# Optimization experiments

Hardware: AMD Instinct MI355X
Metric: run time of the kernel (lower is better)

Reference implementation:

```python
import jax, jax.numpy as jnp
import numpy as np

B, S, D, H, O = 8, 4096, 512, 512, 512
NS, NC, SD = 4, 4, 8
CLIP, TEMP, SUP_SCALE, SUP_EPS, LN_EPS = 3.0, 1.0, 1.0, 1e-4, 1e-5


def _ln(x, w, b):
    m = jnp.mean(x, -1, keepdims=True)
    v = jnp.mean((x - m) ** 2, -1, keepdims=True)
    return (x - m) * jax.lax.rsqrt(v + LN_EPS) * w + b


def _lin(x, w, b):
    return x @ w.T + b


def setup_inputs() -> dict:
    key = jax.random.key(0)
    ks = iter(jax.random.split(key, 32))

    def W(shape):
        return 0.02 * jax.random.normal(next(ks), shape, jnp.float32)

    inp = {}
    inp['x'] = jax.random.normal(next(ks), (B, S, D), jnp.float32)
    inp['sb_norm_w'] = jnp.ones((D,), jnp.float32)
    inp['sb_norm_b'] = jnp.zeros((D,), jnp.float32)
    inp['sb_proj_w'] = W((NS, D)); inp['sb_proj_b'] = jnp.zeros((NS,), jnp.float32)
    inp['sb_sum_w'] = W((SD, 4)); inp['sb_sum_b'] = jnp.zeros((SD,), jnp.float32)
    inp['cb_norm_w'] = jnp.ones((D,), jnp.float32)
    inp['cb_norm_b'] = jnp.zeros((D,), jnp.float32)
    inp['cb_proj_w'] = W((NC, D)); inp['cb_proj_b'] = jnp.zeros((NC,), jnp.float32)
    inp['cb_sum_w'] = W((SD, 4)); inp['cb_sum_b'] = jnp.zeros((SD,), jnp.float32)
    inp['vn_norm_w'] = jnp.ones((D,), jnp.float32)
    inp['vn_norm_b'] = jnp.zeros((D,), jnp.float32)
    inp['vn_w1'] = W((H, D)); inp['vn_b1'] = jnp.zeros((H,), jnp.float32)
    inp['vn_w2'] = W((O, H)); inp['vn_b2'] = jnp.zeros((O,), jnp.float32)
    inp['un_norm_w'] = jnp.ones((D,), jnp.float32)
    inp['un_norm_b'] = jnp.zeros((D,), jnp.float32)
    inp['un_w1'] = W((H, D)); inp['un_b1'] = jnp.zeros((H,), jnp.float32)
    inp['un_w2'] = W((1, H)); inp['un_b2'] = jnp.zeros((1,), jnp.float32)
    inp['en_w'] = W((H, 1)); inp['en_b'] = jnp.zeros((H,), jnp.float32)
    inp['pr_w'] = W((H, 1)); inp['pr_b'] = jnp.zeros((H,), jnp.float32)
    inp['rs_w'] = W((H, 1)); inp['rs_b'] = jnp.zeros((H,), jnp.float32)
    inp['ssp_w'] = W((H, SD)); inp['ssp_b'] = jnp.zeros((H,), jnp.float32)
    inp['csp_w'] = W((H, SD)); inp['csp_b'] = jnp.zeros((H,), jnp.float32)
    inp['out_w'] = W((O, O + 5 * H)); inp['out_b'] = jnp.zeros((O,), jnp.float32)
    inp['support_logits'] = jnp.zeros((NS,), jnp.float32)
    inp['conflict_weights'] = jnp.ones((NC,), jnp.float32)
    inp['drive_bias'] = jnp.zeros((1,), jnp.float32)
    inp['bias_resistance'] = jnp.zeros((1,), jnp.float32)
    inp['update_threshold'] = jnp.ones((1,), jnp.float32)
    inp['eml_gamma'] = jnp.full((1,), 0.3, jnp.float32)
    inp['eml_lambda'] = jnp.ones((1,), jnp.float32)
    inp['eml_bias'] = jnp.zeros((1,), jnp.float32)
    return inp


def reference(x, sb_norm_w, sb_norm_b, sb_proj_w, sb_proj_b, sb_sum_w, sb_sum_b,
              cb_norm_w, cb_norm_b, cb_proj_w, cb_proj_b, cb_sum_w, cb_sum_b,
              vn_norm_w, vn_norm_b, vn_w1, vn_b1, vn_w2, vn_b2,
              un_norm_w, un_norm_b, un_w1, un_b1, un_w2, un_b2,
              en_w, en_b, pr_w, pr_b, rs_w, rs_b,
              ssp_w, ssp_b, csp_w, csp_b, out_w, out_b,
              support_logits, conflict_weights, drive_bias, bias_resistance,
              update_threshold, eml_gamma, eml_lambda, eml_bias):
    # Support bank: LN -> Linear -> softplus(+eps) -> stats -> summary Linear
    sf = jax.nn.softplus(_lin(_ln(x, sb_norm_w, sb_norm_b), sb_proj_w, sb_proj_b)) + SUP_EPS  # [B,S,NS]
    ls = jnp.log(sf)
    s_seed = jnp.concatenate([
        sf.mean(-1, keepdims=True), sf.std(-1, keepdims=True),
        ls.mean(-1, keepdims=True), ls.max(-1, keepdims=True)], -1)
    ss = _lin(s_seed, sb_sum_w, sb_sum_b)  # [B,S,SD]
    # Conflict bank
    cf = jax.nn.softplus(_lin(_ln(x, cb_norm_w, cb_norm_b), cb_proj_w, cb_proj_b))  # [B,S,NC]
    c_seed = jnp.concatenate([
        cf.mean(-1, keepdims=True), cf.std(-1, keepdims=True),
        cf.max(-1, keepdims=True), cf.min(-1, keepdims=True)], -1)
    cs = _lin(c_seed, cb_sum_w, cb_sum_b)  # [B,S,SD]
    # Drive / resistance
    sw = jax.nn.softmax(support_logits)
    drive = drive_bias + SUP_SCALE * (ls * sw).sum(-1, keepdims=True) / np.sqrt(NS)
    cw = jax.nn.softplus(conflict_weights)
    weighted_conflict = (cf * cw).sum(-1, keepdims=True) / np.sqrt(NC)
    u_h = jax.nn.gelu(_lin(_ln(x, un_norm_w, un_norm_b), un_w1, un_b1), approximate=False)
    uncertainty = jax.nn.softplus(_lin(u_h, un_w2, un_b2))  # [B,S,1]
    resistance = bias_resistance + weighted_conflict + uncertainty
    # EML unit (dim=1): bounded linear drive-resistance balance, warmup_eta=1.0
    e_raw = eml_gamma * drive - eml_lambda * resistance + eml_bias
    energy = CLIP * jnp.tanh(e_raw / CLIP)
    activation = jax.nn.sigmoid(energy / TEMP)
    precision = jax.nn.softplus(energy - update_threshold)
    # Value net
    v_h = jax.nn.gelu(_lin(_ln(x, vn_norm_w, vn_norm_b), vn_w1, vn_b1), approximate=False)
    value = _lin(v_h, vn_w2, vn_b2)  # [B,S,O]
    feats = jnp.concatenate([
        activation * value,
        _lin(energy, en_w, en_b),
        _lin(precision, pr_w, pr_b),
        _lin(resistance, rs_w, rs_b),
        _lin(ss, ssp_w, ssp_b),
        _lin(cs, csp_w, csp_b)], -1)  # [B,S,O+5H]
    return _lin(feats, out_w, out_b)  # [B,S,O]
```

## Files before the change

kernel.cpp:

```cpp
#include <hip/hip_runtime.h>
#include <stdint.h>

typedef unsigned short u16;
typedef __bf16 bf16x8 __attribute__((ext_vector_type(8)));
typedef float f32x4 __attribute__((ext_vector_type(4)));
typedef __attribute__((address_space(1))) void gvoid;
typedef __attribute__((address_space(3))) void lvoid;

#define NTOK 32768

__device__ __forceinline__ u16 f2bf(float f) {
    unsigned u = __float_as_uint(f);
    u += 0x7fffu + ((u >> 16) & 1u);
    return (u16)(u >> 16);
}
__device__ __forceinline__ float softplusf(float x) {
    return fmaxf(x, 0.f) + log1pf(expf(-fabsf(x)));
}
__device__ __forceinline__ float geluf(float x) {
    return 0.5f * x * (1.f + erff(x * 0.7071067811865475f));
}
__device__ __forceinline__ float wave_sum(float v) {
#pragma unroll
    for (int o = 32; o > 0; o >>= 1) v += __shfl_xor(v, o);
    return v;
}
__device__ __forceinline__ float blk_sum(float v) {
    __shared__ float sm[4];
    v = wave_sum(v);
    __syncthreads();
    if ((threadIdx.x & 63) == 0) sm[threadIdx.x >> 6] = v;
    __syncthreads();
    return sm[0] + sm[1] + sm[2] + sm[3];
}

__global__ void k_fold(
    const float* __restrict__ vnw1, const float* __restrict__ vnnw, const float* __restrict__ vnnb, const float* __restrict__ vnb1,
    const float* __restrict__ unw1, const float* __restrict__ unnw, const float* __restrict__ unnb, const float* __restrict__ unb1,
    const float* __restrict__ sbpw, const float* __restrict__ sbpb, const float* __restrict__ sbnw, const float* __restrict__ sbnb,
    const float* __restrict__ cbpw, const float* __restrict__ cbpb, const float* __restrict__ cbnw, const float* __restrict__ cbnb,
    const float* __restrict__ outw, const float* __restrict__ enw, const float* __restrict__ enb,
    const float* __restrict__ prw, const float* __restrict__ prb,
    const float* __restrict__ rsw, const float* __restrict__ rsb,
    const float* __restrict__ sspw, const float* __restrict__ sspb,
    const float* __restrict__ cspw, const float* __restrict__ cspb,
    const float* __restrict__ vnw2, const float* __restrict__ vnb2,
    u16* __restrict__ Astk, float* __restrict__ bstk, float* __restrict__ pb,
    u16* __restrict__ Aow, u16* __restrict__ vnT,
    float* __restrict__ a_en, float* __restrict__ a_pr, float* __restrict__ a_rs,
    float* __restrict__ b_vo, float* __restrict__ c_cn, float* __restrict__ Mss, float* __restrict__ Mcs)
{
    const int b = blockIdx.x, t = threadIdx.x;
    if (b < 1024) {
        const float *w1, *nw, *nb; float bias;
        if (b < 512) { w1 = vnw1 + (size_t)b * 512; nw = vnnw; nb = vnnb; bias = vnb1[b]; }
        else { int r = b - 512; w1 = unw1 + (size_t)r * 512; nw = unnw; nb = unnb; bias = unb1[r]; }
        float part = 0.f;
        for (int d = t; d < 512; d += 256) {
            float wv = w1[d];
            Astk[(size_t)b * 512 + d] = f2bf(wv * nw[d]);
            part += wv * nb[d];
        }
        float s = blk_sum(part);
        if (t == 0) bstk[b] = bias + s;
    } else if (b < 1032) {
        int j = b - 1024;
        const float *pw, *nw, *nb; float bias;
        if (j < 4) { pw = sbpw + j * 512; nw = sbnw; nb = sbnb; bias = sbpb[j]; }
        else { pw = cbpw + (j - 4) * 512; nw = cbnw; nb = cbnb; bias = cbpb[j - 4]; }
        float part = 0.f;
        for (int d = t; d < 512; d += 256) {
            float wv = pw[d];
            Astk[(size_t)(1024 + j) * 512 + d] = f2bf(wv * nw[d]);
            part += wv * nb[d];
        }
        float s = blk_sum(part);
        if (t == 0) pb[j] = bias + s;
    } else if (b < 1152) {
        for (int d = t; d < 512; d += 256) Astk[(size_t)b * 512 + d] = 0;
    } else if (b < 1664) {
        int i = b - 1152;
        const float* ow = outw + (size_t)i * 3072;
        float pen = 0, ppr = 0, prs = 0, pbv = 0, pcc = 0;
        float pms[8], pmc[8];
#pragma unroll
        for (int k = 0; k < 8; k++) { pms[k] = 0.f; pmc[k] = 0.f; }
        for (int h = t; h < 512; h += 256) {
            float o0 = ow[h];        Aow[(size_t)i * 512 + h] = f2bf(o0); pbv += o0 * vnb2[h];
            float o1 = ow[512 + h];  pen += o1 * enw[h]; pcc += o1 * enb[h];
            float o2 = ow[1024 + h]; ppr += o2 * prw[h]; pcc += o2 * prb[h];
            float o3 = ow[1536 + h]; prs += o3 * rsw[h]; pcc += o3 * rsb[h];
            float o4 = ow[2048 + h]; pcc += o4 * sspb[h];
            float o5 = ow[2560 + h]; pcc += o5 * cspb[h];
#pragma unroll
            for (int k = 0; k < 8; k++) { pms[k] += o4 * sspw[h * 8 + k]; pmc[k] += o5 * cspw[h * 8 + k]; }
        }
        float r;
        r = blk_sum(pen); if (t == 0) a_en[i] = r;
        r = blk_sum(ppr); if (t == 0) a_pr[i] = r;
        r = blk_sum(prs); if (t == 0) a_rs[i] = r;
        r = blk_sum(pbv); if (t == 0) b_vo[i] = r;
        r = blk_sum(pcc); if (t == 0) c_cn[i] = r;
        for (int k = 0; k < 8; k++) { r = blk_sum(pms[k]); if (t == 0) Mss[i * 8 + k] = r; }
        for (int k = 0; k < 8; k++) { r = blk_sum(pmc[k]); if (t == 0) Mcs[i * 8 + k] = r; }
    } else {
        int hrow = b - 1664;
        for (int o = t; o < 512; o += 256)
            vnT[(size_t)hrow * 512 + o] = f2bf(vnw2[(size_t)o * 512 + hrow]);
    }
}

__device__ __forceinline__ void gemm_tile(const u16* __restrict__ Ab, int lda,
                                          const u16* __restrict__ Bb, int ldb,
                                          int K, u16* lA, u16* lB, f32x4 (&acc)[4][4])
{
    const int t = threadIdx.x;
    const int w = t >> 6, l = t & 63;
    const int lrow = l >> 3;
    const int lcol = (l & 7) * 8;
    const int wr = ((w >> 1) << 6), wc = ((w & 1) << 6);
    const int frow = l & 15, fk = ((l >> 4) << 3);
    for (int kt = 0; kt < K; kt += 64) {
#pragma unroll
        for (int i = 0; i < 4; i++) {
            const int chunk = i * 4 + w;
            const int row = chunk * 8 + lrow;
            const u16* ga = Ab + (size_t)row * lda + kt + lcol;
            const u16* gb = Bb + (size_t)row * ldb + kt + lcol;
            __builtin_amdgcn_global_load_lds((gvoid*)const_cast<u16*>(ga),
                                             (lvoid*)(lA + chunk * 512), 16, 0, 0);
            __builtin_amdgcn_global_load_lds((gvoid*)const_cast<u16*>(gb),
                                             (lvoid*)(lB + chunk * 512), 16, 0, 0);
        }
        __syncthreads();
#pragma unroll
        for (int ks = 0; ks < 2; ks++) {
            bf16x8 af[4], bfv[4];
#pragma unroll
            for (int rt = 0; rt < 4; rt++)
                af[rt] = *(const bf16x8*)(lA + (wr + rt * 16 + frow) * 64 + ks * 32 + fk);
#pragma unroll
            for (int ct = 0; ct < 4; ct++)
                bfv[ct] = *(const bf16x8*)(lB + (wc + ct * 16 + frow) * 64 + ks * 32 + fk);
#pragma unroll
            for (int rt = 0; rt < 4; rt++)
#pragma unroll
                for (int ct = 0; ct < 4; ct++)
                    acc[rt][ct] = __builtin_amdgcn_mfma_f32_16x16x32_bf16(af[rt], bfv[ct], acc[rt][ct], 0, 0, 0);
        }
        __syncthreads();
    }
}

__global__ __launch_bounds__(256, 2) void k_gemm_wvo(const u16* __restrict__ A, const u16* __restrict__ Bm,
                                                     u16* __restrict__ C)
{
    __shared__ u16 lA[8192], lB[8192];
    const f32x4 zero = {0.f, 0.f, 0.f, 0.f};
    f32x4 acc[4][4];
#pragma unroll
    for (int a = 0; a < 4; a++)
#pragma unroll
        for (int c = 0; c < 4; c++) acc[a][c] = zero;
    const u16* Ab = A + (size_t)blockIdx.y * 128 * 512;
    const u16* Bb = Bm + (size_t)blockIdx.x * 128 * 512;
    gemm_tile(Ab, 512, Bb, 512, 512, lA, lB, acc);
    const int t = threadIdx.x, w = t >> 6, l = t & 63;
    const int rbase = blockIdx.y * 128 + ((w >> 1) << 6);
    const int cbase = blockIdx.x * 128 + ((w & 1) << 6);
    const int lr = ((l >> 4) << 2), lc = l & 15;
#pragma unroll
    for (int rt = 0; rt < 4; rt++)
#pragma unroll
        for (int ct = 0; ct < 4; ct++)
#pragma unroll
            for (int j = 0; j < 4; j++)
                C[(size_t)(rbase + rt * 16 + lr + j) * 512 + cbase + ct * 16 + lc] = f2bf(acc[rt][ct][j]);
}

__global__ void k_token(const float* __restrict__ x, u16* __restrict__ Ybf)
{
    const int w = threadIdx.x >> 6, l = threadIdx.x & 63;
    const int n = blockIdx.x * 4 + w;
    const float* xr = x + (size_t)n * 512;
    float4 xa = *(const float4*)(xr + 4 * l);
    float4 xb = *(const float4*)(xr + 256 + 4 * l);
    float v[8] = {xa.x, xa.y, xa.z, xa.w, xb.x, xb.y, xb.z, xb.w};
    float s1 = 0.f, s2 = 0.f;
#pragma unroll
    for (int c = 0; c < 8; c++) { s1 += v[c]; s2 += v[c] * v[c]; }
    s1 = wave_sum(s1); s2 = wave_sum(s2);
    const float mean = s1 * (1.f / 512.f);
    const float var = s2 * (1.f / 512.f) - mean * mean;
    const float rstd = rsqrtf(var + 1e-5f);
    float y[8];
#pragma unroll
    for (int c = 0; c < 8; c++) y[c] = (v[c] - mean) * rstd;
    *(ushort4*)(Ybf + (size_t)n * 512 + 4 * l) = make_ushort4(f2bf(y[0]), f2bf(y[1]), f2bf(y[2]), f2bf(y[3]));
    *(ushort4*)(Ybf + (size_t)n * 512 + 256 + 4 * l) = make_ushort4(f2bf(y[4]), f2bf(y[5]), f2bf(y[6]), f2bf(y[7]));
}

__global__ void k_bank(const float* __restrict__ wp, const float* __restrict__ pb,
                       const float* __restrict__ sbsw, const float* __restrict__ sbsb,
                       const float* __restrict__ cbsw, const float* __restrict__ cbsb,
                       const float* __restrict__ suplog, const float* __restrict__ confw,
                       const float* __restrict__ drvb,
                       float* __restrict__ wss, float* __restrict__ wcs, float* __restrict__ wdw)
{
    const int n = blockIdx.x * 256 + threadIdx.x;
    float4 p0 = *(const float4*)(wp + (size_t)n * 8);
    float4 p1 = *(const float4*)(wp + (size_t)n * 8 + 4);
    float p[8] = {p0.x, p0.y, p0.z, p0.w, p1.x, p1.y, p1.z, p1.w};
    float sf[4], lsv[4], cf[4];
#pragma unroll
    for (int j = 0; j < 4; j++) {
        sf[j] = softplusf(p[j]) + 1e-4f;
        lsv[j] = logf(sf[j]);
        cf[j] = softplusf(p[j + 4]);
    }
    const float smn = 0.25f * (sf[0] + sf[1] + sf[2] + sf[3]);
    float sd = 0.f;
#pragma unroll
    for (int j = 0; j < 4; j++) sd += (sf[j] - smn) * (sf[j] - smn);
    const float sstd = sqrtf(0.25f * sd);
    const float lmn = 0.25f * (lsv[0] + lsv[1] + lsv[2] + lsv[3]);
    const float lmx = fmaxf(fmaxf(lsv[0], lsv[1]), fmaxf(lsv[2], lsv[3]));
    const float cmn = 0.25f * (cf[0] + cf[1] + cf[2] + cf[3]);
    float cd = 0.f;
#pragma unroll
    for (int j = 0; j < 4; j++) cd += (cf[j] - cmn) * (cf[j] - cmn);
    const float cstd = sqrtf(0.25f * cd);
    const float cmx = fmaxf(fmaxf(cf[0], cf[1]), fmaxf(cf[2], cf[3]));
    const float cmi = fminf(fminf(cf[0], cf[1]), fminf(cf[2], cf[3]));
    float seed_s[4] = {smn, sstd, lmn, lmx};
    float seed_c[4] = {cmn, cstd, cmx, cmi};
    float a4[8], b4[8];
#pragma unroll
    for (int k = 0; k < 8; k++) {
        float a = sbsb[k], b2 = cbsb[k];
#pragma unroll
        for (int j = 0; j < 4; j++) { a += sbsw[k * 4 + j] * seed_s[j]; b2 += cbsw[k * 4 + j] * seed_c[j]; }
        a4[k] = a; b4[k] = b2;
    }
    *(float4*)(wss + (size_t)n * 8)     = make_float4(a4[0], a4[1], a4[2], a4[3]);
    *(float4*)(wss + (size_t)n * 8 + 4) = make_float4(a4[4], a4[5], a4[6], a4[7]);
    *(float4*)(wcs + (size_t)n * 8)     = make_float4(b4[0], b4[1], b4[2], b4[3]);
    *(float4*)(wcs + (size_t)n * 8 + 4) = make_float4(b4[4], b4[5], b4[6], b4[7]);
    float mx = fmaxf(fmaxf(suplog[0], suplog[1]), fmaxf(suplog[2], suplog[3]));
    float e[4], se = 0.f;
#pragma unroll
    for (int j = 0; j < 4; j++) { e[j] = expf(suplog[j] - mx); se += e[j]; }
    float dv = 0.f, wcv = 0.f;
#pragma unroll
    for (int j = 0; j < 4; j++) { dv += lsv[j] * (e[j] / se); wcv += cf[j] * softplusf(confw[j]); }
    wdw[(size_t)n * 2 + 0] = drvb[0] + 0.5f * dv;
    wdw[(size_t)n * 2 + 1] = 0.5f * wcv;
    (void)pb;
}

__global__ __launch_bounds__(256, 2) void k_gemm1(const u16* __restrict__ Y, const u16* __restrict__ Ast,
                                                  const float* __restrict__ bstk, const float* __restrict__ pb,
                                                  u16* __restrict__ H, float* __restrict__ wp)
{
    __shared__ u16 lA[8192], lB[8192];
    const f32x4 zero = {0.f, 0.f, 0.f, 0.f};
    f32x4 acc[4][4];
#pragma unroll
    for (int a = 0; a < 4; a++)
#pragma unroll
        for (int c = 0; c < 4; c++) acc[a][c] = zero;
    const int nwg = gridDim.x * gridDim.y;
    const int lin = blockIdx.y * gridDim.x + blockIdx.x;
    const int swz = (lin & 7) * (nwg >> 3) + (lin >> 3);
    const int by = swz / gridDim.x, bx = swz % gridDim.x;
    const u16* Ab = Y + (size_t)by * 128 * 512;
    const u16* Bb = Ast + (size_t)bx * 128 * 512;
    gemm_tile(Ab, 512, Bb, 512, 512, lA, lB, acc);
    const int t = threadIdx.x, w = t >> 6, l = t & 63;
    const int rbase = by * 128 + ((w >> 1) << 6);
    const int cbase0 = ((w & 1) << 6);
    const int lr = ((l >> 4) << 2), lc = l & 15;
    if (bx == 8) {
        if ((w & 1) == 0 && lc < 8) {
            const float bv = pb[lc];
#pragma unroll
            for (int rt = 0; rt < 4; rt++)
#pragma unroll
                for (int j = 0; j < 4; j++) {
                    const int n = rbase + rt * 16 + lr + j;
                    wp[(size_t)n * 8 + lc] = acc[rt][0][j] + bv;
                }
        }
        return;
    }
#pragma unroll
    for (int ct = 0; ct < 4; ct++) {
        const int col = bx * 128 + cbase0 + ct * 16 + lc;
        const float bv = bstk[col];
#pragma unroll
        for (int rt = 0; rt < 4; rt++)
#pragma unroll
            for (int j = 0; j < 4; j++) {
                const int n = rbase + rt * 16 + lr + j;
                H[(size_t)n * 1024 + col] = f2bf(geluf(acc[rt][ct][j] + bv));
            }
    }
}

__global__ void k_scal(const u16* __restrict__ H, const float* __restrict__ unw2, const float* __restrict__ unb2,
                       const float* __restrict__ biasres, const float* __restrict__ emlg,
                       const float* __restrict__ emll, const float* __restrict__ emlb,
                       const float* __restrict__ updthr,
                       const float* __restrict__ wdw, float* __restrict__ wsc)
{
    const int w = threadIdx.x >> 6, l = threadIdx.x & 63;
    const int n = blockIdx.x * 4 + w;
    const u16* hr = H + (size_t)n * 1024 + 512 + 8 * l;
    float4 rawv = *(const float4*)hr;
    const unsigned* pu = (const unsigned*)&rawv;
    const float* uw = unw2 + 8 * l;
    float dot = 0.f;
#pragma unroll
    for (int c = 0; c < 4; c++) {
        unsigned word = pu[c];
        dot += __uint_as_float(word << 16) * uw[2 * c];
        dot += __uint_as_float(word & 0xffff0000u) * uw[2 * c + 1];
    }
    dot = wave_sum(dot);
    if (l == 0) {
        const float unc = softplusf(dot + unb2[0]);
        const float drive = wdw[(size_t)n * 2 + 0];
        const float res = biasres[0] + wdw[(size_t)n * 2 + 1] + unc;
        const float er = emlg[0] * drive - emll[0] * res + emlb[0];
        const float energy = 3.f * tanhf(er * (1.f / 3.f));
        const float act = 1.f / (1.f + expf(-energy));
        const float prc = softplusf(energy - updthr[0]);
        wsc[(size_t)n * 4 + 0] = act;
        wsc[(size_t)n * 4 + 1] = energy;
        wsc[(size_t)n * 4 + 2] = prc;
        wsc[(size_t)n * 4 + 3] = res;
    }
}

__global__ __launch_bounds__(256, 2) void k_gemm2(const u16* __restrict__ H, const u16* __restrict__ Wvo,
    const float* __restrict__ wsc, const float* __restrict__ wss, const float* __restrict__ wcs,
    const float* __restrict__ a_en, const float* __restrict__ a_pr, const float* __restrict__ a_rs,
    const float* __restrict__ b_vo, const float* __restrict__ c_cn,
    const float* __restrict__ Mss, const float* __restrict__ Mcs,
    const float* __restrict__ outb, float* __restrict__ out)
{
    __shared__ u16 lA[8192], lB[8192];
    const f32x4 zero = {0.f, 0.f, 0.f, 0.f};
    f32x4 acc[4][4];
#pragma unroll
    for (int a = 0; a < 4; a++)
#pragma unroll
        for (int c = 0; c < 4; c++) acc[a][c] = zero;
    const int nwg = gridDim.x * gridDim.y;
    const int lin = blockIdx.y * gridDim.x + blockIdx.x;
    const int swz = (lin & 7) * (nwg >> 3) + (lin >> 3);
    const int by = swz / gridDim.x, bx = swz % gridDim.x;
    const u16* Ab = H + (size_t)by * 128 * 1024;
    const u16* Bb = Wvo + (size_t)bx * 128 * 512;
    gemm_tile(Ab, 1024, Bb, 512, 512, lA, lB, acc);
    const int t = threadIdx.x, w = t >> 6, l = t & 63;
    const int rbase = by * 128 + ((w >> 1) << 6);
    const int cbase = bx * 128 + ((w & 1) << 6);
    const int lr = ((l >> 4) << 2), lc = l & 15;
    float bvo4[4], aen4[4], apr4[4], ars4[4], cc4[4], ms4[4][8], mc4[4][8];
#pragma unroll
    for (int ct = 0; ct < 4; ct++) {
        const int i = cbase + ct * 16 + lc;
        bvo4[ct] = b_vo[i]; aen4[ct] = a_en[i]; apr4[ct] = a_pr[i]; ars4[ct] = a_rs[i];
        cc4[ct] = c_cn[i] + outb[i];
#pragma unroll
        for (int k = 0; k < 8; k++) { ms4[ct][k] = Mss[i * 8 + k]; mc4[ct][k] = Mcs[i * 8 + k]; }
    }
#pragma unroll
    for (int rt = 0; rt < 4; rt++)
#pragma unroll
        for (int j = 0; j < 4; j++) {
            const int n = rbase + rt * 16 + lr + j;
            const float act = wsc[(size_t)n * 4 + 0];
            const float eng = wsc[(size_t)n * 4 + 1];
            const float prc = wsc[(size_t)n * 4 + 2];
            const float res = wsc[(size_t)n * 4 + 3];
            float sv[8], cv[8];
#pragma unroll
            for (int k = 0; k < 8; k++) { sv[k] = wss[(size_t)n * 8 + k]; cv[k] = wcs[(size_t)n * 8 + k]; }
#pragma unroll
            for (int ct = 0; ct < 4; ct++) {
                const int i = cbase + ct * 16 + lc;
                float o = act * (acc[rt][ct][j] + bvo4[ct]) + eng * aen4[ct] + prc * apr4[ct]
                        + res * ars4[ct] + cc4[ct];
#pragma unroll
                for (int k = 0; k < 8; k++) o += ms4[ct][k] * sv[k] + mc4[ct][k] * cv[k];
                out[(size_t)n * 512 + i] = o;
            }
        }
}

extern "C" void kernel_launch(void* const* d_in, const int* in_sizes, int n_in,
                              void* d_out, int out_size, void* d_ws, size_t ws_size,
                              hipStream_t stream)
{
    const float* x       = (const float*)d_in[0];
    const float* sbnw    = (const float*)d_in[1];
    const float* sbnb    = (const float*)d_in[2];
    const float* sbpw    = (const float*)d_in[3];
    const float* sbpb    = (const float*)d_in[4];
    const float* sbsw    = (const float*)d_in[5];
    const float* sbsb    = (const float*)d_in[6];
    const float* cbnw    = (const float*)d_in[7];
    const float* cbnb    = (const float*)d_in[8];
    const float* cbpw    = (const float*)d_in[9];
    const float* cbpb    = (const float*)d_in[10];
    const float* cbsw    = (const float*)d_in[11];
    const float* cbsb    = (const float*)d_in[12];
    const float* vnnw    = (const float*)d_in[13];
    const float* vnnb    = (const float*)d_in[14];
    const float* vnw1    = (const float*)d_in[15];
    const float* vnb1    = (const float*)d_in[16];
    const float* vnw2    = (const float*)d_in[17];
    const float* vnb2    = (const float*)d_in[18];
    const float* unnw    = (const float*)d_in[19];
    const float* unnb    = (const float*)d_in[20];
    const float* unw1    = (const float*)d_in[21];
    const float* unb1    = (const float*)d_in[22];
    const float* unw2    = (const float*)d_in[23];
    const float* unb2    = (const float*)d_in[24];
    const float* enw     = (const float*)d_in[25];
    const float* enb     = (const float*)d_in[26];
    const float* prw     = (const float*)d_in[27];
    const float* prb     = (const float*)d_in[28];
    const float* rsw     = (const float*)d_in[29];
    const float* rsb     = (const float*)d_in[30];
    const float* sspw    = (const float*)d_in[31];
    const float* sspb    = (const float*)d_in[32];
    const float* cspw    = (const float*)d_in[33];
    const float* cspb    = (const float*)d_in[34];
    const float* outw    = (const float*)d_in[35];
    const float* outb    = (const float*)d_in[36];
    const float* suplog  = (const float*)d_in[37];
    const float* confw   = (const float*)d_in[38];
    const float* drvb    = (const float*)d_in[39];
    const float* biasres = (const float*)d_in[40];
    const float* updthr  = (const float*)d_in[41];
    const float* emlg    = (const float*)d_in[42];
    const float* emll    = (const float*)d_in[43];
    const float* emlb    = (const float*)d_in[44];
    float* out = (float*)d_out;
    (void)in_sizes; (void)n_in; (void)out_size; (void)ws_size;

    char* wsp = (char*)d_ws;
    size_t off = 0;
    auto alloc = [&](size_t bytes) { char* p = wsp + off; off = (off + bytes + 255) & ~(size_t)255; return p; };
    u16*  Ybf  = (u16*)alloc((size_t)NTOK * 512 * 2);
    u16*  Hbf  = (u16*)alloc((size_t)NTOK * 1024 * 2);
    u16*  Astk = (u16*)alloc(1152 * 512 * 2);
    float* bstk = (float*)alloc(1024 * 4);
    float* pb   = (float*)alloc(8 * 4);
    u16*  Aow  = (u16*)alloc(512 * 512 * 2);
    u16*  vnT  = (u16*)alloc(512 * 512 * 2);
    u16*  Wvo  = (u16*)alloc(512 * 512 * 2);
    float* a_en = (float*)alloc(512 * 4);
    float* a_pr = (float*)alloc(512 * 4);
    float* a_rs = (float*)alloc(512 * 4);
    float* b_vo = (float*)alloc(512 * 4);
    float* c_cn = (float*)alloc(512 * 4);
    float* Mss  = (float*)alloc(512 * 8 * 4);
    float* Mcs  = (float*)alloc(512 * 8 * 4);
    float* wp   = (float*)alloc((size_t)NTOK * 8 * 4);
    float* wss  = (float*)alloc((size_t)NTOK * 8 * 4);
    float* wcs  = (float*)alloc((size_t)NTOK * 8 * 4);
    float* wdw  = (float*)alloc((size_t)NTOK * 2 * 4);
    float* wsc  = (float*)alloc((size_t)NTOK * 4 * 4);

    k_fold<<<2176, 256, 0, stream>>>(vnw1, vnnw, vnnb, vnb1, unw1, unnw, unnb, unb1,
                                     sbpw, sbpb, sbnw, sbnb, cbpw, cbpb, cbnw, cbnb,
                                     outw, enw, enb, prw, prb, rsw, rsb, sspw, sspb, cspw, cspb,
                                     vnw2, vnb2,
                                     Astk, bstk, pb, Aow, vnT, a_en, a_pr, a_rs, b_vo, c_cn, Mss, Mcs);
    k_gemm_wvo<<<dim3(4, 4), 256, 0, stream>>>(Aow, vnT, Wvo);
    k_token<<<NTOK / 4, 256, 0, stream>>>(x, Ybf);
    k_gemm1<<<dim3(9, 256), 256, 0, stream>>>(Ybf, Astk, bstk, pb, Hbf, wp);
    k_bank<<<NTOK / 256, 256, 0, stream>>>(wp, pb, sbsw, sbsb, cbsw, cbsb, suplog, confw, drvb,
                                           wss, wcs, wdw);
    k_scal<<<NTOK / 4, 256, 0, stream>>>(Hbf, unw2, unb2, biasres, emlg, emll, emlb, updthr, wdw, wsc);
    k_gemm2<<<dim3(4, 256), 256, 0, stream>>>(Hbf, Wvo, wsc, wss, wcs, a_en, a_pr, a_rs, b_vo, c_cn,
                                              Mss, Mcs, outb, out);
}
```

Baseline: 175.4 us.

## Double-buffer GEMM LDS tiles with XOR swizzle, stage epilogue, fuse bank kernel

The shared GEMM tile loop now uses two LDS buffers, so the loads for the next K-slice are issued while MFMAs run on the current one. An XOR swizzle is applied to the LDS column layout to cut bank conflicts on fragment reads. k_gemm1 now stages its GELU output in LDS and writes H with coalesced 16-byte stores instead of scattered 2-byte stores. The per-token bank statistics kernel is folded into k_scal's lane-0 path, removing one launch and the wdw round trip. The cost is doubled LDS (64KB per block), which may lower occupancy, plus serial work on a single lane in k_scal.

```diff
diff --git a/kernel.cpp b/kernel.cpp
--- a/kernel.cpp
+++ b/kernel.cpp
@@ -110,44 +110,64 @@
     }
 }
 
+__device__ __forceinline__ void gt_stage(const u16* __restrict__ A_, int lda,
+                                         const u16* __restrict__ B_, int ldb, int kt,
+                                         u16* dA, u16* dB, int w, int lrow, int lcol)
+{
+#pragma unroll
+    for (int i = 0; i < 4; i++) {
+        const int chunk = i * 4 + w;
+        const int row = chunk * 8 + lrow;
+        __builtin_amdgcn_global_load_lds((gvoid*)const_cast<u16*>(A_ + (size_t)row * lda + kt + lcol),
+                                         (lvoid*)(dA + chunk * 512), 16, 0, 0);
+        __builtin_amdgcn_global_load_lds((gvoid*)const_cast<u16*>(B_ + (size_t)row * ldb + kt + lcol),
+                                         (lvoid*)(dB + chunk * 512), 16, 0, 0);
+    }
+}
+
+__device__ __forceinline__ void gt_compute(const u16* lA, const u16* lB, f32x4 (&acc)[4][4],
+                                           int wr, int wc, int frow, int fk, int sw)
+{
+#pragma unroll
+    for (int ks = 0; ks < 2; ks++) {
+        bf16x8 af[4], bfv[4];
+        const int c = (ks * 32 + fk);
+#pragma unroll
+        for (int rt = 0; rt < 4; rt++)
+            af[rt] = *(const bf16x8*)(lA + (wr + rt * 16 + frow) * 64 + (c ^ sw));
+#pragma unroll
+        for (int ct = 0; ct < 4; ct++)
+            bfv[ct] = *(const bf16x8*)(lB + (wc + ct * 16 + frow) * 64 + (c ^ sw));
+#pragma unroll
+        for (int rt = 0; rt < 4; rt++)
+#pragma unroll
+            for (int ct = 0; ct < 4; ct++)
+                acc[rt][ct] = __builtin_amdgcn_mfma_f32_16x16x32_bf16(af[rt], bfv[ct], acc[rt][ct], 0, 0, 0);
+    }
+}
+
 __device__ __forceinline__ void gemm_tile(const u16* __restrict__ Ab, int lda,
                                           const u16* __restrict__ Bb, int ldb,
-                                          int K, u16* lA, u16* lB, f32x4 (&acc)[4][4])
+                                          int K, u16* sm, f32x4 (&acc)[4][4])
 {
     const int t = threadIdx.x;
     const int w = t >> 6, l = t & 63;
     const int lrow = l >> 3;
-    const int lcol = (l & 7) * 8;
+    const int lcol = ((l ^ (((l >> 3) & 3) << 1)) & 7) * 8;
     const int wr = ((w >> 1) << 6), wc = ((w & 1) << 6);
     const int frow = l & 15, fk = ((l >> 4) << 3);
-    for (int kt = 0; kt < K; kt += 64) {
-#pragma unroll
-        for (int i = 0; i < 4; i++) {
-            const int chunk = i * 4 + w;
-            const int row = chunk * 8 + lrow;
-            const u16* ga = Ab + (size_t)row * lda + kt + lcol;
-            const u16* gb = Bb + (size_t)row * ldb + kt + lcol;
-            __builtin_amdgcn_global_load_lds((gvoid*)const_cast<u16*>(ga),
-                                             (lvoid*)(lA + chunk * 512), 16, 0, 0);
-            __builtin_amdgcn_global_load_lds((gvoid*)const_cast<u16*>(gb),
-                                             (lvoid*)(lB + chunk * 512), 16, 0, 0);
-        }
+    const int sw = (frow & 3) << 4;
+    u16* lA0 = sm;          u16* lA1 = sm + 8192;
+    u16* lB0 = sm + 16384;  u16* lB1 = sm + 24576;
+
+    gt_stage(Ab, lda, Bb, ldb, 0, lA0, lB0, w, lrow, lcol);
+    __syncthreads();
+    for (int kt = 0; kt < K; kt += 128) {
+        if (kt + 64 < K) gt_stage(Ab, lda, Bb, ldb, kt + 64, lA1, lB1, w, lrow, lcol);
+        gt_compute(lA0, lB0, acc, wr, wc, frow, fk, sw);
         __syncthreads();
-#pragma unroll
-        for (int ks = 0; ks < 2; ks++) {
-            bf16x8 af[4], bfv[4];
-#pragma unroll
-            for (int rt = 0; rt < 4; rt++)
-                af[rt] = *(const bf16x8*)(lA + (wr + rt * 16 + frow) * 64 + ks * 32 + fk);
-#pragma unroll
-            for (int ct = 0; ct < 4; ct++)
-                bfv[ct] = *(const bf16x8*)(lB + (wc + ct * 16 + frow) * 64 + ks * 32 + fk);
-#pragma unroll
-            for (int rt = 0; rt < 4; rt++)
-#pragma unroll
-                for (int ct = 0; ct < 4; ct++)
-                    acc[rt][ct] = __builtin_amdgcn_mfma_f32_16x16x32_bf16(af[rt], bfv[ct], acc[rt][ct], 0, 0, 0);
-        }
+        if (kt + 128 < K) gt_stage(Ab, lda, Bb, ldb, kt + 128, lA0, lB0, w, lrow, lcol);
+        gt_compute(lA1, lB1, acc, wr, wc, frow, fk, sw);
         __syncthreads();
     }
 }
@@ -155,7 +175,7 @@
 __global__ __launch_bounds__(256, 2) void k_gemm_wvo(const u16* __restrict__ A, const u16* __restrict__ Bm,
                                                      u16* __restrict__ C)
 {
-    __shared__ u16 lA[8192], lB[8192];
+    __shared__ u16 smem[32768];
     const f32x4 zero = {0.f, 0.f, 0.f, 0.f};
     f32x4 acc[4][4];
 #pragma unroll
@@ -164,7 +184,7 @@
         for (int c = 0; c < 4; c++) acc[a][c] = zero;
     const u16* Ab = A + (size_t)blockIdx.y * 128 * 512;
     const u16* Bb = Bm + (size_t)blockIdx.x * 128 * 512;
-    gemm_tile(Ab, 512, Bb, 512, 512, lA, lB, acc);
+    gemm_tile(Ab, 512, Bb, 512, 512, smem, acc);
     const int t = threadIdx.x, w = t >> 6, l = t & 63;
     const int rbase = blockIdx.y * 128 + ((w >> 1) << 6);
     const int cbase = blockIdx.x * 128 + ((w & 1) << 6);
@@ -200,69 +220,11 @@
     *(ushort4*)(Ybf + (size_t)n * 512 + 256 + 4 * l) = make_ushort4(f2bf(y[4]), f2bf(y[5]), f2bf(y[6]), f2bf(y[7]));
 }
 
-__global__ void k_bank(const float* __restrict__ wp, const float* __restrict__ pb,
-                       const float* __restrict__ sbsw, const float* __restrict__ sbsb,
-                       const float* __restrict__ cbsw, const float* __restrict__ cbsb,
-                       const float* __restrict__ suplog, const float* __restrict__ confw,
-                       const float* __restrict__ drvb,
-                       float* __restrict__ wss, float* __restrict__ wcs, float* __restrict__ wdw)
-{
-    const int n = blockIdx.x * 256 + threadIdx.x;
-    float4 p0 = *(const float4*)(wp + (size_t)n * 8);
-    float4 p1 = *(const float4*)(wp + (size_t)n * 8 + 4);
-    float p[8] = {p0.x, p0.y, p0.z, p0.w, p1.x, p1.y, p1.z, p1.w};
-    float sf[4], lsv[4], cf[4];
-#pragma unroll
-    for (int j = 0; j < 4; j++) {
-        sf[j] = softplusf(p[j]) + 1e-4f;
-        lsv[j] = logf(sf[j]);
-        cf[j] = softplusf(p[j + 4]);
-    }
-    const float smn = 0.25f * (sf[0] + sf[1] + sf[2] + sf[3]);
-    float sd = 0.f;
-#pragma unroll
-    for (int j = 0; j < 4; j++) sd += (sf[j] - smn) * (sf[j] - smn);
-    const float sstd = sqrtf(0.25f * sd);
-    const float lmn = 0.25f * (lsv[0] + lsv[1] + lsv[2] + lsv[3]);
-    const float lmx = fmaxf(fmaxf(lsv[0], lsv[1]), fmaxf(lsv[2], lsv[3]));
-    const float cmn = 0.25f * (cf[0] + cf[1] + cf[2] + cf[3]);
-    float cd = 0.f;
-#pragma unroll
-    for (int j = 0; j < 4; j++) cd += (cf[j] - cmn) * (cf[j] - cmn);
-    const float cstd = sqrtf(0.25f * cd);
-    const float cmx = fmaxf(fmaxf(cf[0], cf[1]), fmaxf(cf[2], cf[3]));
-    const float cmi = fminf(fminf(cf[0], cf[1]), fminf(cf[2], cf[3]));
-    float seed_s[4] = {smn, sstd, lmn, lmx};
-    float seed_c[4] = {cmn, cstd, cmx, cmi};
-    float a4[8], b4[8];
-#pragma unroll
-    for (int k = 0; k < 8; k++) {
-        float a = sbsb[k], b2 = cbsb[k];
-#pragma unroll
-        for (int j = 0; j < 4; j++) { a += sbsw[k * 4 + j] * seed_s[j]; b2 += cbsw[k * 4 + j] * seed_c[j]; }
-        a4[k] = a; b4[k] = b2;
-    }
-    *(float4*)(wss + (size_t)n * 8)     = make_float4(a4[0], a4[1], a4[2], a4[3]);
-    *(float4*)(wss + (size_t)n * 8 + 4) = make_float4(a4[4], a4[5], a4[6], a4[7]);
-    *(float4*)(wcs + (size_t)n * 8)     = make_float4(b4[0], b4[1], b4[2], b4[3]);
-    *(float4*)(wcs + (size_t)n * 8 + 4) = make_float4(b4[4], b4[5], b4[6], b4[7]);
-    float mx = fmaxf(fmaxf(suplog[0], suplog[1]), fmaxf(suplog[2], suplog[3]));
-    float e[4], se = 0.f;
-#pragma unroll
-    for (int j = 0; j < 4; j++) { e[j] = expf(suplog[j] - mx); se += e[j]; }
-    float dv = 0.f, wcv = 0.f;
-#pragma unroll
-    for (int j = 0; j < 4; j++) { dv += lsv[j] * (e[j] / se); wcv += cf[j] * softplusf(confw[j]); }
-    wdw[(size_t)n * 2 + 0] = drvb[0] + 0.5f * dv;
-    wdw[(size_t)n * 2 + 1] = 0.5f * wcv;
-    (void)pb;
-}
-
 __global__ __launch_bounds__(256, 2) void k_gemm1(const u16* __restrict__ Y, const u16* __restrict__ Ast,
                                                   const float* __restrict__ bstk, const float* __restrict__ pb,
                                                   u16* __restrict__ H, float* __restrict__ wp)
 {
-    __shared__ u16 lA[8192], lB[8192];
+    __shared__ u16 smem[32768];
     const f32x4 zero = {0.f, 0.f, 0.f, 0.f};
     f32x4 acc[4][4];
 #pragma unroll
@@ -275,14 +237,14 @@
     const int by = swz / gridDim.x, bx = swz % gridDim.x;
     const u16* Ab = Y + (size_t)by * 128 * 512;
     const u16* Bb = Ast + (size_t)bx * 128 * 512;
-    gemm_tile(Ab, 512, Bb, 512, 512, lA, lB, acc);
+    gemm_tile(Ab, 512, Bb, 512, 512, smem, acc);
     const int t = threadIdx.x, w = t >> 6, l = t & 63;
-    const int rbase = by * 128 + ((w >> 1) << 6);
-    const int cbase0 = ((w & 1) << 6);
+    const int wr = ((w >> 1) << 6), wc = ((w & 1) << 6);
     const int lr = ((l >> 4) << 2), lc = l & 15;
     if (bx == 8) {
         if ((w & 1) == 0 && lc < 8) {
             const float bv = pb[lc];
+            const int rbase = by * 128 + wr;
 #pragma unroll
             for (int rt = 0; rt < 4; rt++)
 #pragma unroll
@@ -295,23 +257,35 @@
     }
 #pragma unroll
     for (int ct = 0; ct < 4; ct++) {
-        const int col = bx * 128 + cbase0 + ct * 16 + lc;
-        const float bv = bstk[col];
-#pragma unroll
-        for (int rt = 0; rt < 4; rt++)
-#pragma unroll
-            for (int j = 0; j < 4; j++) {
-                const int n = rbase + rt * 16 + lr + j;
-                H[(size_t)n * 1024 + col] = f2bf(geluf(acc[rt][ct][j] + bv));
-            }
-    }
-}
-
-__global__ void k_scal(const u16* __restrict__ H, const float* __restrict__ unw2, const float* __restrict__ unb2,
-                       const float* __restrict__ biasres, const float* __restrict__ emlg,
-                       const float* __restrict__ emll, const float* __restrict__ emlb,
-                       const float* __restrict__ updthr,
-                       const float* __restrict__ wdw, float* __restrict__ wsc)
+        const int col = wc + ct * 16 + lc;
+        const float bv = bstk[bx * 128 + col];
+#pragma unroll
+        for (int rt = 0; rt < 4; rt++) {
+            const int row = wr + rt * 16 + lr;
+#pragma unroll
+            for (int j = 0; j < 4; j++)
+                smem[(row + j) * 136 + col] = f2bf(geluf(acc[rt][ct][j] + bv));
+        }
+    }
+    __syncthreads();
+    const size_t gbase = (size_t)(by * 128) * 1024 + bx * 128;
+#pragma unroll
+    for (int jj = 0; jj < 8; jj++) {
+        const int r = jj * 16 + (t >> 4), u = t & 15;
+        bf16x8 vv = *(const bf16x8*)(smem + r * 136 + u * 8);
+        *(bf16x8*)(H + gbase + (size_t)r * 1024 + u * 8) = vv;
+    }
+}
+
+__global__ void k_scal(const u16* __restrict__ H, const float* __restrict__ wp,
+                       const float* __restrict__ unw2, const float* __restrict__ unb2,
+                       const float* __restrict__ sbsw, const float* __restrict__ sbsb,
+                       const float* __restrict__ cbsw, const float* __restrict__ cbsb,
+                       const float* __restrict__ suplog, const float* __restrict__ confw,
+                       const float* __restrict__ drvb, const float* __restrict__ biasres,
+                       const float* __restrict__ emlg, const float* __restrict__ emll,
+                       const float* __restrict__ emlb, const float* __restrict__ updthr,
+                       float* __restrict__ wss, float* __restrict__ wcs, float* __restrict__ wsc)
 {
     const int w = threadIdx.x >> 6, l = threadIdx.x & 63;
     const int n = blockIdx.x * 4 + w;
@@ -328,9 +302,50 @@
     }
     dot = wave_sum(dot);
     if (l == 0) {
+        float4 p0 = *(const float4*)(wp + (size_t)n * 8);
+        float4 p1 = *(const float4*)(wp + (size_t)n * 8 + 4);
+        float p[8] = {p0.x, p0.y, p0.z, p0.w, p1.x, p1.y, p1.z, p1.w};
+        float sf[4], lsv[4], cf[4];
+#pragma unroll
+        for (int j = 0; j < 4; j++) {
+            sf[j] = softplusf(p[j]) + 1e-4f;
+            lsv[j] = logf(sf[j]);
+            cf[j] = softplusf(p[j + 4]);
+        }
+        const float smn = 0.25f * (sf[0] + sf[1] + sf[2] + sf[3]);
+        float sd = 0.f;
+#pragma unroll
+        for (int j = 0; j < 4; j++) sd += (sf[j] - smn) * (sf[j] - smn);
+        const float sstd = sqrtf(0.25f * sd);
+        const float lmn = 0.25f * (lsv[0] + lsv[1] + lsv[2] + lsv[3]);
+        const float lmx = fmaxf(fmaxf(lsv[0], lsv[1]), fmaxf(lsv[2], lsv[3]));
+        const float cmn = 0.25f * (cf[0] + cf[1] + cf[2] + cf[3]);
+        float cd = 0.f;
+#pragma unroll
+        for (int j = 0; j < 4; j++) cd += (cf[j] - cmn) * (cf[j] - cmn);
+        const float cstd = sqrtf(0.25f * cd);
+        const float cmx = fmaxf(fmaxf(cf[0], cf[1]), fmaxf(cf[2], cf[3]));
+        const float cmi = fminf(fminf(cf[0], cf[1]), fminf(cf[2], cf[3]));
+        float seed_s[4] = {smn, sstd, lmn, lmx};
+        float seed_c[4] = {cmn, cstd, cmx, cmi};
+#pragma unroll
+        for (int k = 0; k < 8; k++) {
+            float a = sbsb[k], b2 = cbsb[k];
+#pragma unroll
+            for (int j = 0; j < 4; j++) { a += sbsw[k * 4 + j] * seed_s[j]; b2 += cbsw[k * 4 + j] * seed_c[j]; }
+            wss[(size_t)n * 8 + k] = a;
+            wcs[(size_t)n * 8 + k] = b2;
+        }
+        float mx = fmaxf(fmaxf(suplog[0], suplog[1]), fmaxf(suplog[2], suplog[3]));
+        float e[4], se = 0.f;
+#pragma unroll
+        for (int j = 0; j < 4; j++) { e[j] = expf(suplog[j] - mx); se += e[j]; }
+        float dv = 0.f, wcv = 0.f;
+#pragma unroll
+        for (int j = 0; j < 4; j++) { dv += lsv[j] * (e[j] / se); wcv += cf[j] * softplusf(confw[j]); }
+        const float drive = drvb[0] + 0.5f * dv;
         const float unc = softplusf(dot + unb2[0]);
-        const float drive = wdw[(size_t)n * 2 + 0];
-        const float res = biasres[0] + wdw[(size_t)n * 2 + 1] + unc;
+        const float res = biasres[0] + 0.5f * wcv + unc;
         const float er = emlg[0] * drive - emll[0] * res + emlb[0];
         const float energy = 3.f * tanhf(er * (1.f / 3.f));
         const float act = 1.f / (1.f + expf(-energy));
@@ -349,7 +364,7 @@
     const float* __restrict__ Mss, const float* __restrict__ Mcs,
     const float* __restrict__ outb, float* __restrict__ out)
 {
-    __shared__ u16 lA[8192], lB[8192];
+    __shared__ u16 smem[32768];
     const f32x4 zero = {0.f, 0.f, 0.f, 0.f};
     f32x4 acc[4][4];
 #pragma unroll
@@ -362,7 +377,7 @@
     const int by = swz / gridDim.x, bx = swz % gridDim.x;
     const u16* Ab = H + (size_t)by * 128 * 1024;
     const u16* Bb = Wvo + (size_t)bx * 128 * 512;
-    gemm_tile(Ab, 1024, Bb, 512, 512, lA, lB, acc);
+    gemm_tile(Ab, 1024, Bb, 512, 512, smem, acc);
     const int t = threadIdx.x, w = t >> 6, l = t & 63;
     const int rbase = by * 128 + ((w >> 1) << 6);
     const int cbase = bx * 128 + ((w & 1) << 6);
@@ -473,7 +488,6 @@
     float* wp   = (float*)alloc((size_t)NTOK * 8 * 4);
     float* wss  = (float*)alloc((size_t)NTOK * 8 * 4);
     float* wcs  = (float*)alloc((size_t)NTOK * 8 * 4);
-    float* wdw  = (float*)alloc((size_t)NTOK * 2 * 4);
     float* wsc  = (float*)alloc((size_t)NTOK * 4 * 4);
 
     k_fold<<<2176, 256, 0, stream>>>(vnw1, vnnw, vnnb, vnb1, unw1, unnw, unnb, unb1,
@@ -484,9 +498,9 @@
     k_gemm_wvo<<<dim3(4, 4), 256, 0, stream>>>(Aow, vnT, Wvo);
     k_token<<<NTOK / 4, 256, 0, stream>>>(x, Ybf);
     k_gemm1<<<dim3(9, 256), 256, 0, stream>>>(Ybf, Astk, bstk, pb, Hbf, wp);
-    k_bank<<<NTOK / 256, 256, 0, stream>>>(wp, pb, sbsw, sbsb, cbsw, cbsb, suplog, confw, drvb,
-                                           wss, wcs, wdw);
-    k_scal<<<NTOK / 4, 256, 0, stream>>>(Hbf, unw2, unb2, biasres, emlg, emll, emlb, updthr, wdw, wsc);
+    k_scal<<<NTOK / 4, 256, 0, stream>>>(Hbf, wp, unw2, unb2, sbsw, sbsb, cbsw, cbsb,
+                                         suplog, confw, drvb, biasres, emlg, emll, emlb, updthr,
+                                         wss, wcs, wsc);
     k_gemm2<<<dim3(4, 256), 256, 0, stream>>>(Hbf, Wvo, wsc, wss, wcs, a_en, a_pr, a_rs, b_vo, c_cn,
                                               Mss, Mcs, outb, out);
 }
```

Result: slower. 257.2 us (+46.7%).
